# Kernel tuning notes

Measured on AMD Instinct MI355X. Metric: run time of the kernel, lower is better.

Reference implementation:

```python
import jax, jax.numpy as jnp
import numpy as np

NUM_FIELDS = 40
EMBED_DIM = 16

# Precompute static gather indices equivalent to the two masked_select calls.
# triu mask on a (F, F-1) grid, diagonal=0 -> pairs (i, j) with j >= i.
_tri = np.triu(np.ones((NUM_FIELDS, NUM_FIELDS - 1), dtype=np.int64), 0).astype(bool)
_I0, _J0 = np.nonzero(_tri)  # row-major order matches torch.masked_select
# tril(ones(F, F-1), -1).T -> (F-1, F) mask applied to x.transpose(1, 2).
_trl = np.tril(np.ones((NUM_FIELDS, NUM_FIELDS - 1), dtype=np.int64), -1).T.astype(bool)
_I1, _J1 = np.nonzero(_trl)  # indices into the transposed view
I0 = jnp.asarray(_I0); J0 = jnp.asarray(_J0)
I1 = jnp.asarray(_I1); J1 = jnp.asarray(_J1)


def setup_inputs() -> dict:
    key = jax.random.key(0)
    bs = 2048
    inputs = jax.random.normal(key, (bs, NUM_FIELDS * (NUM_FIELDS - 1) * EMBED_DIM), dtype=jnp.float32)
    return {"inputs": inputs}


def reference(inputs):
    bs = inputs.shape[0]
    F = NUM_FIELDS
    # [bs, F, F-1, D]
    x = inputs.reshape(bs, F, F - 1, -1)
    # emb0 = masked_select(x, triu_mask): gather pairs in row-major order
    emb0 = x[:, I0, J0, :]            # [bs, P, D], P = F*(F-1)/2
    # emb1 = masked_select(x.transpose(1,2), tril_mask): xt[b,a,c,:] = x[b,c,a,:]
    emb1 = x[:, J1, I1, :]            # [bs, P, D]
    # (emb0*emb1).view(bs,-1).sum(-1)
    return jnp.einsum('bpd,bpd->b', emb0, emb1)
```

## Files before the change

kernel.cpp:

```cpp
#include <hip/hip_runtime.h>


#define NF 40
#define NC 39
#define ED 16
#define NPAIRS 780
#define ROW_FLOATS (NF * NC * ED)
#define NTASKS (NPAIRS * 4)
#define NTHREADS 512

struct Tables {
    unsigned short a_glob[NPAIRS];
    unsigned short b_slot[NPAIRS];
    unsigned short b_glob[NPAIRS];
};

static constexpr Tables make_tables() {
    Tables t{};
    int p = 0;
    for (int i = 0; i < NC; ++i)
        for (int j = i; j < NC; ++j, ++p) {
            t.a_glob[p] = (unsigned short)(i * NC + j);
            t.b_slot[p] = (unsigned short)((j + 1) * j / 2 + i);
        }
    for (int g = 1; g < NF; ++g)
        for (int c = 0; c < g; ++c)
            t.b_glob[g * (g - 1) / 2 + c] = (unsigned short)(g * NC + c);
    return t;
}

__constant__ Tables c_tab = make_tables();

__global__ __launch_bounds__(NTHREADS) void ffm_interact_kernel(
        const float* __restrict__ x, float* __restrict__ out) {
    __shared__ float ldsb[NPAIRS * ED];
    const int n = blockIdx.x;
    const int tid = threadIdx.x;
    const float4* __restrict__ base4 =
        (const float4*)(x + (size_t)n * ROW_FLOATS);
    float4* lds4 = (float4*)ldsb;

    #pragma unroll
    for (int t = tid; t < NTASKS; t += NTHREADS) {
        const int s = t >> 2;
        const int q = t & 3;
        lds4[s * 4 + q] = base4[(int)c_tab.b_glob[s] * 4 + q];
    }
    __syncthreads();

    float acc = 0.0f;
    #pragma unroll
    for (int t = tid; t < NTASKS; t += NTHREADS) {
        const int p = t >> 2;
        const int q = t & 3;
        const float4 a = base4[(int)c_tab.a_glob[p] * 4 + q];
        const float4 b = lds4[(int)c_tab.b_slot[p] * 4 + q];
        acc = fmaf(a.x, b.x, acc);
        acc = fmaf(a.y, b.y, acc);
        acc = fmaf(a.z, b.z, acc);
        acc = fmaf(a.w, b.w, acc);
    }

    #pragma unroll
    for (int off = 32; off > 0; off >>= 1)
        acc += __shfl_down(acc, off, 64);

    __shared__ float wave_sum[NTHREADS / 64];
    const int lane = threadIdx.x & 63;
    const int wid  = threadIdx.x >> 6;
    if (lane == 0) wave_sum[wid] = acc;
    __syncthreads();
    if (tid == 0) {
        float s = 0.0f;
        #pragma unroll
        for (int w = 0; w < NTHREADS / 64; ++w) s += wave_sum[w];
        out[n] = s;
    }
}

extern "C" void kernel_launch(void* const* d_in, const int* in_sizes, int n_in,
                              void* d_out, int out_size, void* d_ws, size_t ws_size,
                              hipStream_t stream) {
    const float* x = (const float*)d_in[0];
    float* out = (float*)d_out;
    const int bs = in_sizes[0] / ROW_FLOATS;
    ffm_interact_kernel<<<bs, NTHREADS, 0, stream>>>(x, out);
}
```

Baseline: 274.9 us.

## Drop LDS staging; load both operands directly with packed index table

```diff
diff --git a/kernel.cpp b/kernel.cpp
--- a/kernel.cpp
+++ b/kernel.cpp
@@ -7,73 +7,69 @@
 #define NPAIRS 780
 #define ROW_FLOATS (NF * NC * ED)
 #define NTASKS (NPAIRS * 4)
-#define NTHREADS 512
+#define NTH 512
+#define TRIPS ((NTASKS + NTH - 1) / NTH)
 
-struct Tables {
-    unsigned short a_glob[NPAIRS];
-    unsigned short b_slot[NPAIRS];
-    unsigned short b_glob[NPAIRS];
-};
+typedef float f32x4 __attribute__((ext_vector_type(4)));
 
-static constexpr Tables make_tables() {
-    Tables t{};
+struct PairPack { unsigned int pk[NPAIRS]; };
+
+static constexpr PairPack make_pk() {
+    PairPack t{};
     int p = 0;
     for (int i = 0; i < NC; ++i)
-        for (int j = i; j < NC; ++j, ++p) {
-            t.a_glob[p] = (unsigned short)(i * NC + j);
-            t.b_slot[p] = (unsigned short)((j + 1) * j / 2 + i);
-        }
-    for (int g = 1; g < NF; ++g)
-        for (int c = 0; c < g; ++c)
-            t.b_glob[g * (g - 1) / 2 + c] = (unsigned short)(g * NC + c);
+        for (int j = i; j < NC; ++j, ++p)
+            t.pk[p] = (unsigned)(i * NC + j)
+                    | ((unsigned)((j + 1) * NC + i) << 16);
     return t;
 }
 
-__constant__ Tables c_tab = make_tables();
+__constant__ PairPack c_tab = make_pk();
 
-__global__ __launch_bounds__(NTHREADS) void ffm_interact_kernel(
+__global__ __launch_bounds__(NTH) void ffm_interact_kernel(
         const float* __restrict__ x, float* __restrict__ out) {
-    __shared__ float ldsb[NPAIRS * ED];
     const int n = blockIdx.x;
     const int tid = threadIdx.x;
-    const float4* __restrict__ base4 =
-        (const float4*)(x + (size_t)n * ROW_FLOATS);
-    float4* lds4 = (float4*)ldsb;
+    const int q = tid & 3;
+    const f32x4* __restrict__ base4 =
+        (const f32x4*)(x + (size_t)n * ROW_FLOATS);
 
+    unsigned idx[TRIPS];
     #pragma unroll
-    for (int t = tid; t < NTASKS; t += NTHREADS) {
-        const int s = t >> 2;
-        const int q = t & 3;
-        lds4[s * 4 + q] = base4[(int)c_tab.b_glob[s] * 4 + q];
+    for (int k = 0; k < TRIPS; ++k) {
+        int p = (tid + k * NTH) >> 2;
+        idx[k] = c_tab.pk[p < NPAIRS ? p : 0];
     }
-    __syncthreads();
+
+    f32x4 av[TRIPS], bv[TRIPS];
+    #pragma unroll
+    for (int k = 0; k < TRIPS; ++k)
+        av[k] = __builtin_nontemporal_load(&base4[(int)(idx[k] & 0xffffu) * 4 + q]);
+    #pragma unroll
+    for (int k = 0; k < TRIPS; ++k)
+        bv[k] = __builtin_nontemporal_load(&base4[(int)(idx[k] >> 16) * 4 + q]);
 
     float acc = 0.0f;
     #pragma unroll
-    for (int t = tid; t < NTASKS; t += NTHREADS) {
-        const int p = t >> 2;
-        const int q = t & 3;
-        const float4 a = base4[(int)c_tab.a_glob[p] * 4 + q];
-        const float4 b = lds4[(int)c_tab.b_slot[p] * 4 + q];
-        acc = fmaf(a.x, b.x, acc);
-        acc = fmaf(a.y, b.y, acc);
-        acc = fmaf(a.z, b.z, acc);
-        acc = fmaf(a.w, b.w, acc);
+    for (int k = 0; k < TRIPS; ++k) {
+        const float m = ((tid + k * NTH) < NTASKS) ? 1.0f : 0.0f;
+        acc = fmaf(m * av[k][0], bv[k][0], acc);
+        acc = fmaf(m * av[k][1], bv[k][1], acc);
+        acc = fmaf(m * av[k][2], bv[k][2], acc);
+        acc = fmaf(m * av[k][3], bv[k][3], acc);
     }
 
     #pragma unroll
     for (int off = 32; off > 0; off >>= 1)
         acc += __shfl_down(acc, off, 64);
 
-    __shared__ float wave_sum[NTHREADS / 64];
-    const int lane = threadIdx.x & 63;
-    const int wid  = threadIdx.x >> 6;
-    if (lane == 0) wave_sum[wid] = acc;
+    __shared__ float wave_sum[NTH / 64];
+    if ((tid & 63) == 0) wave_sum[tid >> 6] = acc;
     __syncthreads();
     if (tid == 0) {
         float s = 0.0f;
         #pragma unroll
-        for (int w = 0; w < NTHREADS / 64; ++w) s += wave_sum[w];
+        for (int w = 0; w < NTH / 64; ++w) s += wave_sum[w];
         out[n] = s;
     }
 }
@@ -84,5 +80,5 @@
     const float* x = (const float*)d_in[0];
     float* out = (float*)d_out;
     const int bs = in_sizes[0] / ROW_FLOATS;
-    ffm_interact_kernel<<<bs, NTHREADS, 0, stream>>>(x, out);
+    ffm_interact_kernel<<<bs, NTH, 0, stream>>>(x, out);
 }
```

Result: faster. 257.0 us (-6.5%).
